# Kernel optimization log

Hardware: AMD Instinct MI355X
Metric: run time of the kernel (lower is better)

The kernel has to match this reference:

```python
import jax, jax.numpy as jnp
import numpy as np

P = 16  # patch size
D = 768  # embedding dim


def setup_inputs() -> dict:
    key = jax.random.key(0)
    k_img, k_w, k_b = jax.random.split(key, 3)
    B, H, W, C = 64, 224, 224, 3
    image = jax.random.normal(k_img, (B, H, W, C), dtype=jnp.float32)
    patch_dim = P * P * C  # 768
    # Keras Dense default: glorot_uniform kernel, zeros bias
    limit = np.sqrt(6.0 / (patch_dim + D)).astype(np.float32)
    W_proj = jax.random.uniform(k_w, (patch_dim, D), dtype=jnp.float32,
                                minval=-limit, maxval=limit)
    b_proj = jnp.zeros((D,), dtype=jnp.float32)
    return {"image": image, "W_proj": W_proj, "b_proj": b_proj}


def reference(image, W_proj, b_proj):
    B, H, W, C = image.shape
    nh, nw = H // P, W // P
    # Fused im2col replacing the per-patch slicing loop:
    # [B,H,W,C] -> [B, nh, P, nw, P, C] -> [B, nh, nw, P, P, C] -> [B, nh*nw, P*P*C]
    # Row-major (p_i, p_j) patch order matches the original nested loop, and
    # flatten of a [B,P,P,C] slice matches the (P,P,C) raveling here.
    patches = image.reshape(B, nh, P, nw, P, C)
    patches = patches.transpose(0, 1, 3, 2, 4, 5).reshape(B, nh * nw, P * P * C)
    # Dense + exact GELU (tf.keras.activations.gelu default approximate=False)
    x = jnp.einsum('bnp,pd->bnd', patches, W_proj) + b_proj
    return jax.nn.gelu(x, approximate=False)
```

## Files before the change

### kernel.cpp

```cpp
#include <hip/hip_runtime.h>
#include <hip/hip_bf16.h>
#include <math.h>

#define MM 12544
#define KK 768
#define NN 768
#define BM 64
#define BN 256
#define NKS 24
#define MT 196
#define NT 3
#define N64 12

#define A_BLOCKS (MT * NKS)
#define W_BLOCKS (N64 * NKS)
#define FRAG_BYTES 1024
#define KSTRIDE (4 * FRAG_BYTES)
#define PANEL_BYTES (NKS * KSTRIDE)

typedef __bf16 v8bf __attribute__((ext_vector_type(8)));
typedef float  v4f  __attribute__((ext_vector_type(4)));

__global__ __launch_bounds__(256) void pack_kernel(const float* __restrict__ img,
                                                   const float* __restrict__ w,
                                                   __hip_bfloat16* __restrict__ apack,
                                                   __hip_bfloat16* __restrict__ wpack) {
    const int tid  = threadIdx.x;
    const int l    = tid & 63;
    const int fi   = tid >> 6;
    const int l_lo = l & 15;
    const int l_hi = l >> 4;

    union { __hip_bfloat16 h[8]; uint4 u; } o;

    if (blockIdx.x < A_BLOCKS) {
        const int bid = blockIdx.x;
        const int mt  = bid / NKS;
        const int ks  = bid - mt * NKS;
        const int m   = mt * 64 + fi * 16 + l_lo;
        const int k0  = ks * 32 + l_hi * 8;
        const int b   = m / 196;
        const int pm  = m - b * 196;
        const int pr  = pm / 14;
        const int pc  = pm - pr * 14;
        const int i   = k0 / 48;
        const int rem = k0 - i * 48;
        const float* src = img + (size_t)(((b * 224 + pr * 16 + i) * 224 + pc * 16) * 3 + rem);
        float4 f0 = *(const float4*)src;
        float4 f1 = *(const float4*)(src + 4);
        o.h[0] = __float2bfloat16(f0.x); o.h[1] = __float2bfloat16(f0.y);
        o.h[2] = __float2bfloat16(f0.z); o.h[3] = __float2bfloat16(f0.w);
        o.h[4] = __float2bfloat16(f1.x); o.h[5] = __float2bfloat16(f1.y);
        o.h[6] = __float2bfloat16(f1.z); o.h[7] = __float2bfloat16(f1.w);
        ((uint4*)apack)[(size_t)((mt * NKS + ks) * 4 + fi) * 64 + l] = o.u;
    } else {
        const int bid = blockIdx.x - A_BLOCKS;
        const int n64 = bid / NKS;
        const int ks  = bid - n64 * NKS;
        const int col = n64 * 64 + fi * 16 + l_lo;
        const int k0  = ks * 32 + l_hi * 8;
        float f[8];
#pragma unroll
        for (int j = 0; j < 8; j++) f[j] = w[(size_t)(k0 + j) * NN + col];
#pragma unroll
        for (int j = 0; j < 8; j++) o.h[j] = __float2bfloat16(f[j]);
        ((uint4*)wpack)[(size_t)((n64 * NKS + ks) * 4 + fi) * 64 + l] = o.u;
    }
}

__device__ __forceinline__ float gelu_fast(float x) {
    float t2 = 1.5957691216057308f * x * (1.0f + 0.044715f * x * x);
    float e  = __expf(t2);
    float r  = __builtin_amdgcn_rcpf(e + 1.0f);
    return x - x * r;
}

__global__ __launch_bounds__(256, 3) void gemm_reg(const __hip_bfloat16* __restrict__ apack,
                                                   const __hip_bfloat16* __restrict__ wpack,
                                                   const float* __restrict__ bias,
                                                   float* __restrict__ out) {
    const int h   = blockIdx.x;
    const int xcd = h & 7;
    const int jj  = h >> 3;
    const int u   = (xcd < 4 ? xcd * 74 : 296 + (xcd - 4) * 73) + jj;
    const int nt  = u % 3;
    const int mt  = u / 3;

    const int tid  = threadIdx.x;
    const int lane = tid & 63;
    const int wave = tid >> 6;
    const int col  = lane & 15;
    const int quad = lane >> 4;

    const char* pA = (const char*)apack + (size_t)mt * PANEL_BYTES + lane * 16;
    const char* pB = (const char*)wpack + (size_t)(nt * 4 + wave) * PANEL_BYTES + lane * 16;

    v4f acc[4][4];
    const v4f vzero = {0.f, 0.f, 0.f, 0.f};
#pragma unroll
    for (int a = 0; a < 4; a++)
#pragma unroll
        for (int c = 0; c < 4; c++) acc[a][c] = vzero;

    v8bf aR[2][4], bR[2][4];
#pragma unroll
    for (int mi = 0; mi < 4; mi++) aR[0][mi] = *(const v8bf*)(pA + mi * FRAG_BYTES);
#pragma unroll
    for (int ni = 0; ni < 4; ni++) bR[0][ni] = *(const v8bf*)(pB + ni * FRAG_BYTES);

#pragma unroll
    for (int ks = 0; ks < NKS; ks++) {
        const int cur = ks & 1;
        if (ks + 1 < NKS) {
            const char* qA = pA + (size_t)(ks + 1) * KSTRIDE;
            const char* qB = pB + (size_t)(ks + 1) * KSTRIDE;
#pragma unroll
            for (int mi = 0; mi < 4; mi++)
                aR[cur ^ 1][mi] = *(const v8bf*)(qA + mi * FRAG_BYTES);
#pragma unroll
            for (int ni = 0; ni < 4; ni++)
                bR[cur ^ 1][ni] = *(const v8bf*)(qB + ni * FRAG_BYTES);
        }
#pragma unroll
        for (int mi = 0; mi < 4; mi++)
#pragma unroll
            for (int ni = 0; ni < 4; ni++)
                acc[mi][ni] = __builtin_amdgcn_mfma_f32_16x16x32_bf16(
                    aR[cur][mi], bR[cur][ni], acc[mi][ni], 0, 0, 0);
    }

#pragma unroll
    for (int ni = 0; ni < 4; ni++) {
        int n    = nt * BN + wave * 64 + ni * 16 + col;
        float bv = bias[n];
#pragma unroll
        for (int mi = 0; mi < 4; mi++) {
            int rowb = mt * BM + mi * 16 + quad * 4;
            float* po = out + (size_t)rowb * NN + n;
#pragma unroll
            for (int rg = 0; rg < 4; rg++) {
                float x = acc[mi][ni][rg] + bv;
                po[(size_t)rg * NN] = gelu_fast(x);
            }
        }
    }
}

extern "C" void kernel_launch(void* const* d_in, const int* in_sizes, int n_in,
                              void* d_out, int out_size, void* d_ws, size_t ws_size,
                              hipStream_t stream) {
    const float* img   = (const float*)d_in[0];
    const float* wproj = (const float*)d_in[1];
    const float* bias  = (const float*)d_in[2];
    float* out = (float*)d_out;

    __hip_bfloat16* apack = (__hip_bfloat16*)d_ws;
    __hip_bfloat16* wpack = (__hip_bfloat16*)((char*)d_ws + (size_t)MM * KK * 2);

    pack_kernel<<<dim3(A_BLOCKS + W_BLOCKS), dim3(256), 0, stream>>>(
        img, wproj, apack, wpack);
    gemm_reg<<<dim3(MT * NT), dim3(256), 0, stream>>>(apack, wpack, bias, out);
}
```

Measured before the change: 119.8 us.

## Fuse image im2col/bf16 conversion into GEMM and widen N tile to 384

```diff
diff --git a/kernel.cpp b/kernel.cpp
--- a/kernel.cpp
+++ b/kernel.cpp
@@ -6,66 +6,29 @@
 #define KK 768
 #define NN 768
 #define BM 64
-#define BN 256
+#define BN 384
 #define NKS 24
 #define MT 196
-#define NT 3
-#define N64 12
+#define NT 2
+#define NBLK (MT * NT)
 
-#define A_BLOCKS (MT * NKS)
-#define W_BLOCKS (N64 * NKS)
-#define FRAG_BYTES 1024
-#define KSTRIDE (4 * FRAG_BYTES)
-#define PANEL_BYTES (NKS * KSTRIDE)
+#define W_CHUNKS (48 * NKS * 64)
 
 typedef __bf16 v8bf __attribute__((ext_vector_type(8)));
 typedef float  v4f  __attribute__((ext_vector_type(4)));
 
-__global__ __launch_bounds__(256) void pack_kernel(const float* __restrict__ img,
-                                                   const float* __restrict__ w,
-                                                   __hip_bfloat16* __restrict__ apack,
-                                                   __hip_bfloat16* __restrict__ wpack) {
-    const int tid  = threadIdx.x;
-    const int l    = tid & 63;
-    const int fi   = tid >> 6;
-    const int l_lo = l & 15;
-    const int l_hi = l >> 4;
-
+__global__ __launch_bounds__(256) void wpack_kernel(const float* __restrict__ w,
+                                                    __hip_bfloat16* __restrict__ wpack) {
+    int tid  = blockIdx.x * 256 + threadIdx.x;
+    int lane = tid & 63;
+    int c16  = (tid >> 6) % 48;
+    int ks   = tid / (64 * 48);
+    int n    = c16 * 16 + (lane & 15);
+    int k0   = ks * 32 + (lane >> 4) * 8;
     union { __hip_bfloat16 h[8]; uint4 u; } o;
-
-    if (blockIdx.x < A_BLOCKS) {
-        const int bid = blockIdx.x;
-        const int mt  = bid / NKS;
-        const int ks  = bid - mt * NKS;
-        const int m   = mt * 64 + fi * 16 + l_lo;
-        const int k0  = ks * 32 + l_hi * 8;
-        const int b   = m / 196;
-        const int pm  = m - b * 196;
-        const int pr  = pm / 14;
-        const int pc  = pm - pr * 14;
-        const int i   = k0 / 48;
-        const int rem = k0 - i * 48;
-        const float* src = img + (size_t)(((b * 224 + pr * 16 + i) * 224 + pc * 16) * 3 + rem);
-        float4 f0 = *(const float4*)src;
-        float4 f1 = *(const float4*)(src + 4);
-        o.h[0] = __float2bfloat16(f0.x); o.h[1] = __float2bfloat16(f0.y);
-        o.h[2] = __float2bfloat16(f0.z); o.h[3] = __float2bfloat16(f0.w);
-        o.h[4] = __float2bfloat16(f1.x); o.h[5] = __float2bfloat16(f1.y);
-        o.h[6] = __float2bfloat16(f1.z); o.h[7] = __float2bfloat16(f1.w);
-        ((uint4*)apack)[(size_t)((mt * NKS + ks) * 4 + fi) * 64 + l] = o.u;
-    } else {
-        const int bid = blockIdx.x - A_BLOCKS;
-        const int n64 = bid / NKS;
-        const int ks  = bid - n64 * NKS;
-        const int col = n64 * 64 + fi * 16 + l_lo;
-        const int k0  = ks * 32 + l_hi * 8;
-        float f[8];
 #pragma unroll
-        for (int j = 0; j < 8; j++) f[j] = w[(size_t)(k0 + j) * NN + col];
-#pragma unroll
-        for (int j = 0; j < 8; j++) o.h[j] = __float2bfloat16(f[j]);
-        ((uint4*)wpack)[(size_t)((n64 * NKS + ks) * 4 + fi) * 64 + l] = o.u;
-    }
+    for (int j = 0; j < 8; j++) o.h[j] = __float2bfloat16(w[(size_t)(k0 + j) * NN + n]);
+    ((uint4*)wpack)[tid] = o.u;
 }
 
 __device__ __forceinline__ float gelu_fast(float x) {
@@ -75,67 +38,113 @@
     return x - x * r;
 }
 
-__global__ __launch_bounds__(256, 3) void gemm_reg(const __hip_bfloat16* __restrict__ apack,
-                                                   const __hip_bfloat16* __restrict__ wpack,
-                                                   const float* __restrict__ bias,
-                                                   float* __restrict__ out) {
-    const int h   = blockIdx.x;
-    const int xcd = h & 7;
-    const int jj  = h >> 3;
-    const int u   = (xcd < 4 ? xcd * 74 : 296 + (xcd - 4) * 73) + jj;
-    const int nt  = u % 3;
-    const int mt  = u / 3;
+__global__ __launch_bounds__(256, 2) void gemm_fused(const float* __restrict__ img,
+                                                     const __hip_bfloat16* __restrict__ wpack,
+                                                     const float* __restrict__ bias,
+                                                     float* __restrict__ out) {
+    const int h  = blockIdx.x;
+    const int u  = (h & 7) * 49 + (h >> 3);
+    const int mt = u >> 1;
+    const int nt = u & 1;
 
     const int tid  = threadIdx.x;
     const int lane = tid & 63;
     const int wave = tid >> 6;
-    const int col  = lane & 15;
-    const int quad = lane >> 4;
+    const int l_lo = lane & 15;
+    const int l_hi = lane >> 4;
 
-    const char* pA = (const char*)apack + (size_t)mt * PANEL_BYTES + lane * 16;
-    const char* pB = (const char*)wpack + (size_t)(nt * 4 + wave) * PANEL_BYTES + lane * 16;
+    int aoff[4];
+#pragma unroll
+    for (int mi = 0; mi < 4; mi++) {
+        int m  = mt * 64 + mi * 16 + l_lo;
+        int b  = m / 196, pm = m - b * 196;
+        int pr = pm / 14, pc = pm - pr * 14;
+        aoff[mi] = ((b * 224 + pr * 16) * 224 + pc * 16) * 3;
+    }
+    int rowoff[3];
+#pragma unroll
+    for (int s = 0; s < 3; s++) {
+        int k0 = s * 32 + l_hi * 8;
+        int i  = (k0 >= 48) ? 1 : 0;
+        rowoff[s] = i * 672 + (k0 - i * 48);
+    }
 
-    v4f acc[4][4];
+    const int bbase = (nt * 24 + wave * 6) * 64 + lane;
+    const uint4* wp = (const uint4*)wpack;
+
+    v4f acc[4][6];
     const v4f vzero = {0.f, 0.f, 0.f, 0.f};
 #pragma unroll
     for (int a = 0; a < 4; a++)
 #pragma unroll
-        for (int c = 0; c < 4; c++) acc[a][c] = vzero;
+        for (int c = 0; c < 6; c++) acc[a][c] = vzero;
 
-    v8bf aR[2][4], bR[2][4];
-#pragma unroll
-    for (int mi = 0; mi < 4; mi++) aR[0][mi] = *(const v8bf*)(pA + mi * FRAG_BYTES);
-#pragma unroll
-    for (int ni = 0; ni < 4; ni++) bR[0][ni] = *(const v8bf*)(pB + ni * FRAG_BYTES);
+    v8bf   aR[2][4];
+    v8bf   bR[2][6];
+    float4 fA[4][2];
+
+#define LOADA(ks_)                                                            \
+    {   _Pragma("unroll")                                                     \
+        for (int mi = 0; mi < 4; mi++) {                                      \
+            const float* p = img + aoff[mi] + rowoff[(ks_) % 3] + ((ks_) / 3) * 1344; \
+            fA[mi][0] = *(const float4*)p;                                    \
+            fA[mi][1] = *(const float4*)(p + 4);                              \
+        }  }
+
+#define LOADB(ks_, d)                                                         \
+    {   _Pragma("unroll")                                                     \
+        for (int ni = 0; ni < 6; ni++)                                        \
+            bR[d][ni] = *(const v8bf*)&wp[bbase + (ks_) * 3072 + ni * 64];  }
+
+#define CVTA(d)                                                               \
+    {   _Pragma("unroll")                                                     \
+        for (int mi = 0; mi < 4; mi++) {                                      \
+            union { __hip_bfloat16 hh[8]; v8bf v; } t;                        \
+            t.hh[0] = __float2bfloat16(fA[mi][0].x);                          \
+            t.hh[1] = __float2bfloat16(fA[mi][0].y);                          \
+            t.hh[2] = __float2bfloat16(fA[mi][0].z);                          \
+            t.hh[3] = __float2bfloat16(fA[mi][0].w);                          \
+            t.hh[4] = __float2bfloat16(fA[mi][1].x);                          \
+            t.hh[5] = __float2bfloat16(fA[mi][1].y);                          \
+            t.hh[6] = __float2bfloat16(fA[mi][1].z);                          \
+            t.hh[7] = __float2bfloat16(fA[mi][1].w);                          \
+            aR[d][mi] = t.v;                                                  \
+        }  }
+
+#define DOMFMA(d)                                                             \
+    {   __builtin_amdgcn_s_setprio(1);                                        \
+        _Pragma("unroll")                                                     \
+        for (int mi = 0; mi < 4; mi++)                                        \
+            _Pragma("unroll")                                                 \
+            for (int ni = 0; ni < 6; ni++)                                    \
+                acc[mi][ni] = __builtin_amdgcn_mfma_f32_16x16x32_bf16(        \
+                    aR[d][mi], bR[d][ni], acc[mi][ni], 0, 0, 0);              \
+        __builtin_amdgcn_s_setprio(0);  }
+
+    LOADA(0);
+    LOADB(0, 0);
+    CVTA(0);
 
 #pragma unroll
     for (int ks = 0; ks < NKS; ks++) {
         const int cur = ks & 1;
+        const int nxt = cur ^ 1;
         if (ks + 1 < NKS) {
-            const char* qA = pA + (size_t)(ks + 1) * KSTRIDE;
-            const char* qB = pB + (size_t)(ks + 1) * KSTRIDE;
-#pragma unroll
-            for (int mi = 0; mi < 4; mi++)
-                aR[cur ^ 1][mi] = *(const v8bf*)(qA + mi * FRAG_BYTES);
-#pragma unroll
-            for (int ni = 0; ni < 4; ni++)
-                bR[cur ^ 1][ni] = *(const v8bf*)(qB + ni * FRAG_BYTES);
+            LOADA(ks + 1);
+            LOADB(ks + 1, nxt);
         }
-#pragma unroll
-        for (int mi = 0; mi < 4; mi++)
-#pragma unroll
-            for (int ni = 0; ni < 4; ni++)
-                acc[mi][ni] = __builtin_amdgcn_mfma_f32_16x16x32_bf16(
-                    aR[cur][mi], bR[cur][ni], acc[mi][ni], 0, 0, 0);
+        DOMFMA(cur);
+        __builtin_amdgcn_sched_barrier(0);
+        if (ks + 1 < NKS) CVTA(nxt);
     }
 
 #pragma unroll
-    for (int ni = 0; ni < 4; ni++) {
-        int n    = nt * BN + wave * 64 + ni * 16 + col;
+    for (int ni = 0; ni < 6; ni++) {
+        int n    = nt * BN + wave * 96 + ni * 16 + l_lo;
         float bv = bias[n];
 #pragma unroll
         for (int mi = 0; mi < 4; mi++) {
-            int rowb = mt * BM + mi * 16 + quad * 4;
+            int rowb = mt * 64 + mi * 16 + l_hi * 4;
             float* po = out + (size_t)rowb * NN + n;
 #pragma unroll
             for (int rg = 0; rg < 4; rg++) {
@@ -144,6 +153,10 @@
             }
         }
     }
+#undef LOADA
+#undef LOADB
+#undef CVTA
+#undef DOMFMA
 }
 
 extern "C" void kernel_launch(void* const* d_in, const int* in_sizes, int n_in,
@@ -154,10 +167,8 @@
     const float* bias  = (const float*)d_in[2];
     float* out = (float*)d_out;
 
-    __hip_bfloat16* apack = (__hip_bfloat16*)d_ws;
-    __hip_bfloat16* wpack = (__hip_bfloat16*)((char*)d_ws + (size_t)MM * KK * 2);
+    __hip_bfloat16* wpack = (__hip_bfloat16*)d_ws;
 
-    pack_kernel<<<dim3(A_BLOCKS + W_BLOCKS), dim3(256), 0, stream>>>(
-        img, wproj, apack, wpack);
-    gemm_reg<<<dim3(MT * NT), dim3(256), 0, stream>>>(apack, wpack, bias, out);
+    wpack_kernel<<<dim3(W_CHUNKS / 256), dim3(256), 0, stream>>>(wproj, wpack);
+    gemm_fused<<<dim3(NBLK), dim3(256), 0, stream>>>(img, wpack, bias, out);
 }
```

Measured after the change: 141.5 us. 1.18x slower.
